# Kernel optimization log

Measured on AMD Instinct MI355X. Metric: run time of the kernel, lower is better.

## Reference

```python
import jax, jax.numpy as jnp
import numpy as np

N_EMBD = 384
N_HEAD = 6
HEAD_SIZE = N_EMBD // N_HEAD  # 64
B, T = 128, 256
EPS = 1e-5


def setup_inputs() -> dict:
    key = jax.random.key(0)
    ks = jax.random.split(key, 12)
    s = 0.02
    return {
        "x": jax.random.normal(ks[0], (B, T, N_EMBD), dtype=jnp.float32),
        "Wk": jax.random.normal(ks[1], (N_EMBD, N_EMBD), dtype=jnp.float32) * s,
        "Wq": jax.random.normal(ks[2], (N_EMBD, N_EMBD), dtype=jnp.float32) * s,
        "Wv": jax.random.normal(ks[3], (N_EMBD, N_EMBD), dtype=jnp.float32) * s,
        "Wo": jax.random.normal(ks[4], (N_EMBD, N_EMBD), dtype=jnp.float32) * s,
        "bo": jnp.zeros((N_EMBD,), dtype=jnp.float32),
        "W1": jax.random.normal(ks[5], (N_EMBD, 4 * N_EMBD), dtype=jnp.float32) * s,
        "b1": jnp.zeros((4 * N_EMBD,), dtype=jnp.float32),
        "W2": jax.random.normal(ks[6], (4 * N_EMBD, N_EMBD), dtype=jnp.float32) * s,
        "b2": jnp.zeros((N_EMBD,), dtype=jnp.float32),
        "g1": jnp.ones((N_EMBD,), dtype=jnp.float32),
        "be1": jnp.zeros((N_EMBD,), dtype=jnp.float32),
        "g2": jnp.ones((N_EMBD,), dtype=jnp.float32),
        "be2": jnp.zeros((N_EMBD,), dtype=jnp.float32),
    }


def _layernorm(x, g, b):
    mu = jnp.mean(x, axis=-1, keepdims=True)
    var = jnp.var(x, axis=-1, keepdims=True)
    return (x - mu) * jax.lax.rsqrt(var + EPS) * g + b


def _attention(x, Wk, Wq, Wv, Wo, bo):
    Bb, Tt, C = x.shape
    H, D = N_HEAD, HEAD_SIZE
    k = (x @ Wk).reshape(Bb, Tt, H, D).transpose(0, 2, 1, 3)  # (B,H,T,D)
    q = (x @ Wq).reshape(Bb, Tt, H, D).transpose(0, 2, 1, 3)
    v = (x @ Wv).reshape(Bb, Tt, H, D).transpose(0, 2, 1, 3)
    wei = jnp.einsum("bhqd,bhkd->bhqk", q, k) * (D ** -0.5)  # (B,H,T,T)
    mask = jnp.tril(jnp.ones((Tt, Tt), dtype=bool))
    wei = jnp.where(mask, wei, -jnp.inf)
    wei = jax.nn.softmax(wei, axis=-1)
    out = jnp.einsum("bhqk,bhkd->bhqd", wei, v)
    out = out.transpose(0, 2, 1, 3).reshape(Bb, Tt, H * D)
    return out @ Wo + bo


def reference(x, Wk, Wq, Wv, Wo, bo, W1, b1, W2, b2, g1, be1, g2, be2):
    # dropout is identity in eval mode
    h = _layernorm(x, g1, be1)
    x = x + _attention(h, Wk, Wq, Wv, Wo, bo)
    h = _layernorm(x, g2, be2)
    ff = jax.nn.relu(h @ W1 + b1) @ W2 + b2
    return x + ff
```

## Files before the change

### kernel.cpp

```cpp
#include <hip/hip_runtime.h>

typedef unsigned short u16;
typedef short s16x8 __attribute__((ext_vector_type(8)));
typedef float f32x4 __attribute__((ext_vector_type(4)));

__device__ inline u16 f2bf(float f) {
    unsigned u = __float_as_uint(f);
    u += 0x7FFF + ((u >> 16) & 1);
    return (u16)(u >> 16);
}
__device__ inline float bf2f(u16 h) {
    return __uint_as_float((unsigned)h << 16);
}

__device__ inline f32x4 mfma16(s16x8 a, s16x8 b, f32x4 c) {
    return __builtin_amdgcn_mfma_f32_16x16x32_bf16(a, b, c, 0, 0, 0);
}

__device__ __forceinline__ void gl16(const u16* g, u16* l) {
    __builtin_amdgcn_global_load_lds(
        (const __attribute__((address_space(1))) void*)g,
        (__attribute__((address_space(3))) void*)l, 16, 0, 0);
}

__global__ void tcvt_all(const float* __restrict__ Wq, const float* __restrict__ Wk,
                         const float* __restrict__ Wv, const float* __restrict__ Wo,
                         const float* __restrict__ W1, const float* __restrict__ W2,
                         u16* __restrict__ out) {
    int i = blockIdx.x * 256 + threadIdx.x;
    float val;
    if (i < 589824) {
        int q = i / 147456, j = i - q * 147456;
        const float* s = q == 0 ? Wq : q == 1 ? Wk : q == 2 ? Wv : Wo;
        int n = j / 384, k = j - n * 384;
        val = s[k * 384 + n];
    } else if (i < 1179648) {
        int j = i - 589824;
        int n = j / 384, k = j - n * 384;
        val = W1[(size_t)k * 1536 + n];
    } else {
        int j = i - 1179648;
        int n = j / 1536, k = j - n * 1536;
        val = W2[(size_t)k * 384 + n];
    }
    out[i] = f2bf(val);
}

__global__ __launch_bounds__(256) void ln_kernel(const float* __restrict__ x,
                                                 const float* __restrict__ g,
                                                 const float* __restrict__ be,
                                                 u16* __restrict__ out) {
    int lane = threadIdx.x & 63;
    int w = threadIdx.x >> 6;
    int row = blockIdx.x * 4 + w;
    const float* xr = x + (size_t)row * 384;
    float v[6];
    float s = 0.f, sq = 0.f;
#pragma unroll
    for (int i = 0; i < 6; ++i) {
        v[i] = xr[i * 64 + lane];
        s += v[i];
        sq += v[i] * v[i];
    }
#pragma unroll
    for (int m = 1; m < 64; m <<= 1) {
        s += __shfl_xor(s, m);
        sq += __shfl_xor(sq, m);
    }
    float mu = s * (1.0f / 384.0f);
    float var = sq * (1.0f / 384.0f) - mu * mu;
    float rstd = rsqrtf(var + 1e-5f);
    u16* orow = out + (size_t)row * 384;
#pragma unroll
    for (int i = 0; i < 6; ++i) {
        int col = i * 64 + lane;
        orow[col] = f2bf((v[i] - mu) * rstd * g[col] + be[col]);
    }
}

__global__ __launch_bounds__(256) void ln_bf16_kernel(const u16* __restrict__ x,
                                                      const float* __restrict__ g,
                                                      const float* __restrict__ be,
                                                      u16* __restrict__ out) {
    int lane = threadIdx.x & 63;
    int w = threadIdx.x >> 6;
    int row = blockIdx.x * 4 + w;
    const u16* xr = x + (size_t)row * 384;
    bool act = lane < 48;
    float v[8];
    float s = 0.f, sq = 0.f;
    if (act) {
        s16x8 t = *(const s16x8*)&xr[lane * 8];
#pragma unroll
        for (int j = 0; j < 8; ++j) {
            v[j] = bf2f((u16)t[j]);
            s += v[j];
            sq += v[j] * v[j];
        }
    }
#pragma unroll
    for (int m = 1; m < 64; m <<= 1) {
        s += __shfl_xor(s, m);
        sq += __shfl_xor(sq, m);
    }
    float mu = s * (1.0f / 384.0f);
    float var = sq * (1.0f / 384.0f) - mu * mu;
    float rstd = rsqrtf(var + 1e-5f);
    if (act) {
        float4 g0 = *(const float4*)&g[lane * 8];
        float4 g1 = *(const float4*)&g[lane * 8 + 4];
        float4 b0 = *(const float4*)&be[lane * 8];
        float4 b1 = *(const float4*)&be[lane * 8 + 4];
        float gg[8] = {g0.x, g0.y, g0.z, g0.w, g1.x, g1.y, g1.z, g1.w};
        float bb[8] = {b0.x, b0.y, b0.z, b0.w, b1.x, b1.y, b1.z, b1.w};
        u16* orow = out + (size_t)row * 384 + lane * 8;
#pragma unroll
        for (int j = 0; j < 8; ++j)
            orow[j] = f2bf((v[j] - mu) * rstd * gg[j] + bb[j]);
    }
}

template <int BIAS, int RELU, int RES, int RESBF, int OBF16, int NBN>
__global__ __launch_bounds__(512, 4) void gemm_kernel(const u16* __restrict__ A,
                                                      const u16* __restrict__ Bt,
                                                      const float* __restrict__ bias,
                                                      const void* __restrict__ res,
                                                      void* __restrict__ out,
                                                      int M, int N, int K) {
    __shared__ u16 La[2][256 * 32];
    __shared__ u16 Lb[2][128 * 32];
    int tid = threadIdx.x;
    int lane = tid & 63, w = tid >> 6;
    int wm = w >> 1, wn = w & 1;
    int lr = lane & 15, lg = lane >> 4;

    int nwg = gridDim.x;
    int q = nwg >> 3, r = nwg & 7;
    int xcd = blockIdx.x & 7, lin = blockIdx.x >> 3;
    int wg = (xcd < r ? xcd * (q + 1) : r * (q + 1) + (xcd - r) * q) + lin;
    int bx = wg % NBN, by = wg / NBN;
    int m0 = by * 256, n0 = bx * 128;

    int rsub = lane >> 2;
    int gslot = ((lane & 3) ^ ((lane >> 3) & 3)) * 8;
    const u16* pa[2];
    const u16* pb1;
#pragma unroll
    for (int i = 0; i < 2; ++i)
        pa[i] = A + (size_t)(m0 + w * 32 + i * 16 + rsub) * K + gslot;
    pb1 = Bt + (size_t)(n0 + w * 16 + rsub) * K + gslot;

    f32x4 acc[4][4];
    f32x4 zero = {0.f, 0.f, 0.f, 0.f};
#pragma unroll
    for (int mt = 0; mt < 4; ++mt)
#pragma unroll
        for (int nt = 0; nt < 4; ++nt) acc[mt][nt] = zero;

    int sel = (lg ^ ((lr >> 1) & 3)) << 3;
    int nt_steps = K >> 5;

#define STAGE(t, bsel)                                  \
    do {                                                \
        int kc = (t) << 5;                              \
        gl16(pa[0] + kc, &La[bsel][(w * 32) * 32]);     \
        gl16(pa[1] + kc, &La[bsel][(w * 32 + 16) * 32]);\
        gl16(pb1 + kc, &Lb[bsel][(w * 16) * 32]);       \
    } while (0)

    STAGE(0, 0);

    for (int t = 0; t < nt_steps; ++t) {
        asm volatile("s_waitcnt vmcnt(0)" ::: "memory");
        __builtin_amdgcn_s_barrier();
        asm volatile("" ::: "memory");
        if (t + 1 < nt_steps) STAGE(t + 1, (t + 1) & 1);
        const u16* lab = La[t & 1];
        const u16* lbb = Lb[t & 1];
        s16x8 af[4], bfr[4];
#pragma unroll
        for (int mt = 0; mt < 4; ++mt)
            af[mt] = *(const s16x8*)&lab[(wm * 64 + mt * 16 + lr) * 32 + sel];
#pragma unroll
        for (int nt = 0; nt < 4; ++nt)
            bfr[nt] = *(const s16x8*)&lbb[(wn * 64 + nt * 16 + lr) * 32 + sel];
        __builtin_amdgcn_s_setprio(1);
#pragma unroll
        for (int mt = 0; mt < 4; ++mt)
#pragma unroll
            for (int nt = 0; nt < 4; ++nt)
                acc[mt][nt] = mfma16(af[mt], bfr[nt], acc[mt][nt]);
        __builtin_amdgcn_s_setprio(0);
    }
#undef STAGE

#pragma unroll
    for (int mt = 0; mt < 4; ++mt) {
#pragma unroll
        for (int nt = 0; nt < 4; ++nt) {
            int m_base = m0 + wm * 64 + mt * 16 + lg * 4;
            int n = n0 + wn * 64 + nt * 16 + lr;
            float bv = BIAS ? bias[n] : 0.0f;
#pragma unroll
            for (int r2 = 0; r2 < 4; ++r2) {
                size_t idx = (size_t)(m_base + r2) * N + n;
                float val = acc[mt][nt][r2] + bv;
                if (RES) {
                    if (RESBF)
                        val += bf2f(((const u16*)res)[idx]);
                    else
                        val += ((const float*)res)[idx];
                }
                if (RELU) val = fmaxf(val, 0.0f);
                if (OBF16)
                    ((u16*)out)[idx] = f2bf(val);
                else
                    ((float*)out)[idx] = val;
            }
        }
    }
}

__global__ __launch_bounds__(512) void attn_kernel(const u16* __restrict__ qkv,
                                                   u16* __restrict__ aout) {
    __shared__ u16 Kl[256 * 72];
    __shared__ u16 Vt[64 * 264];
    __shared__ u16 Pl[8 * 16 * 264];
    int qt = blockIdx.x, h = blockIdx.y, b = blockIdx.z;
    int tid = threadIdx.x, lane = tid & 63, w = tid >> 6;
    int lr = lane & 15, lg = lane >> 4;
    const u16* qb = qkv + (size_t)b * 256 * 1152;

#pragma unroll
    for (int i = 0; i < 4; ++i) {
        int c = tid + i * 512;
        int t = c >> 3, dch = c & 7;
        *(int4*)&Kl[t * 72 + dch * 8] =
            *(const int4*)(qb + (size_t)t * 1152 + 384 + h * 64 + dch * 8);
        union { int4 v; u16 u[8]; } vv;
        vv.v = *(const int4*)(qb + (size_t)t * 1152 + 768 + h * 64 + dch * 8);
#pragma unroll
        for (int j = 0; j < 8; ++j) Vt[(dch * 8 + j) * 264 + t] = vv.u[j];
    }

    int q0 = qt * 128;
    const u16* qrow = qb + (size_t)(q0 + w * 16 + lr) * 1152 + h * 64;
    s16x8 qf0 = *(const s16x8*)(qrow + lg * 8);
    s16x8 qf1 = *(const s16x8*)(qrow + 32 + lg * 8);

    __syncthreads();

    f32x4 zero = {0.f, 0.f, 0.f, 0.f};
    f32x4 s[16];
#pragma unroll
    for (int nt = 0; nt < 16; ++nt) s[nt] = zero;
#pragma unroll
    for (int nt = 0; nt < 16; ++nt) {
        s16x8 kf0 = *(const s16x8*)&Kl[(nt * 16 + lr) * 72 + lg * 8];
        s16x8 kf1 = *(const s16x8*)&Kl[(nt * 16 + lr) * 72 + 32 + lg * 8];
        s[nt] = mfma16(qf0, kf0, s[nt]);
        s[nt] = mfma16(qf1, kf1, s[nt]);
    }

    int ib = q0 + w * 16 + lg * 4;
    float mx[4] = {-1e30f, -1e30f, -1e30f, -1e30f};
#pragma unroll
    for (int nt = 0; nt < 16; ++nt) {
        int jg = nt * 16 + lr;
#pragma unroll
        for (int r = 0; r < 4; ++r) {
            float val = s[nt][r] * 0.125f;
            val = (jg <= ib + r) ? val : -1e30f;
            s[nt][r] = val;
            mx[r] = fmaxf(mx[r], val);
        }
    }
#pragma unroll
    for (int r = 0; r < 4; ++r) {
        mx[r] = fmaxf(mx[r], __shfl_xor(mx[r], 1));
        mx[r] = fmaxf(mx[r], __shfl_xor(mx[r], 2));
        mx[r] = fmaxf(mx[r], __shfl_xor(mx[r], 4));
        mx[r] = fmaxf(mx[r], __shfl_xor(mx[r], 8));
    }
    float rs[4] = {0.f, 0.f, 0.f, 0.f};
#pragma unroll
    for (int nt = 0; nt < 16; ++nt) {
#pragma unroll
        for (int r = 0; r < 4; ++r) {
            float p = __expf(s[nt][r] - mx[r]);
            s[nt][r] = p;
            rs[r] += p;
        }
    }
#pragma unroll
    for (int r = 0; r < 4; ++r) {
        rs[r] += __shfl_xor(rs[r], 1);
        rs[r] += __shfl_xor(rs[r], 2);
        rs[r] += __shfl_xor(rs[r], 4);
        rs[r] += __shfl_xor(rs[r], 8);
    }
    u16* Pw = &Pl[w * 16 * 264];
#pragma unroll
    for (int nt = 0; nt < 16; ++nt)
#pragma unroll
        for (int r = 0; r < 4; ++r)
            Pw[(lg * 4 + r) * 264 + nt * 16 + lr] = f2bf(s[nt][r]);

    __syncthreads();

    f32x4 o[4];
#pragma unroll
    for (int nt = 0; nt < 4; ++nt) o[nt] = zero;
#pragma unroll
    for (int kc = 0; kc < 8; ++kc) {
        s16x8 pf = *(const s16x8*)&Pw[lr * 264 + kc * 32 + lg * 8];
#pragma unroll
        for (int nt = 0; nt < 4; ++nt) {
            s16x8 vf = *(const s16x8*)&Vt[(nt * 16 + lr) * 264 + kc * 32 + lg * 8];
            o[nt] = mfma16(pf, vf, o[nt]);
        }
    }
    float inv[4];
#pragma unroll
    for (int r = 0; r < 4; ++r) inv[r] = 1.0f / rs[r];
    u16* ob = aout + (size_t)(b * 256 + q0 + w * 16) * 384 + h * 64;
#pragma unroll
    for (int nt = 0; nt < 4; ++nt)
#pragma unroll
        for (int r = 0; r < 4; ++r)
            ob[(size_t)(lg * 4 + r) * 384 + nt * 16 + lr] = f2bf(o[nt][r] * inv[r]);
}

extern "C" void kernel_launch(void* const* d_in, const int* in_sizes, int n_in,
                              void* d_out, int out_size, void* d_ws, size_t ws_size,
                              hipStream_t stream) {
    const float* x   = (const float*)d_in[0];
    const float* Wk  = (const float*)d_in[1];
    const float* Wq  = (const float*)d_in[2];
    const float* Wv  = (const float*)d_in[3];
    const float* Wo  = (const float*)d_in[4];
    const float* bo  = (const float*)d_in[5];
    const float* W1  = (const float*)d_in[6];
    const float* b1  = (const float*)d_in[7];
    const float* W2  = (const float*)d_in[8];
    const float* b2  = (const float*)d_in[9];
    const float* g1  = (const float*)d_in[10];
    const float* be1 = (const float*)d_in[11];
    const float* g2  = (const float*)d_in[12];
    const float* be2 = (const float*)d_in[13];

    char* ws = (char*)d_ws;
    u16* hbuf = (u16*)(ws + 0);
    u16* qkv  = (u16*)(ws + 25165824);
    u16* ao   = (u16*)(ws + 100663296);
    u16* x1   = (u16*)(ws + 125829120);
    u16* ubuf = (u16*)(ws + 25165824);
    u16* wT   = (u16*)(ws + 150994944);
    u16* wqkvT = wT;
    u16* woT   = wT + 442368;
    u16* w1T   = woT + 147456;
    u16* w2T   = w1T + 589824;

    tcvt_all<<<6912, 256, 0, stream>>>(Wq, Wk, Wv, Wo, W1, W2, wT);

    ln_kernel<<<8192, 256, 0, stream>>>(x, g1, be1, hbuf);
    gemm_kernel<0, 0, 0, 0, 1, 9><<<1152, 512, 0, stream>>>(
        hbuf, wqkvT, nullptr, nullptr, qkv, 32768, 1152, 384);
    attn_kernel<<<dim3(2, 6, 128), 512, 0, stream>>>(qkv, ao);
    gemm_kernel<1, 0, 1, 0, 1, 3><<<384, 512, 0, stream>>>(
        ao, woT, bo, x, x1, 32768, 384, 384);
    ln_bf16_kernel<<<8192, 256, 0, stream>>>(x1, g2, be2, hbuf);
    gemm_kernel<1, 1, 0, 0, 1, 12><<<1536, 512, 0, stream>>>(
        hbuf, w1T, b1, nullptr, ubuf, 32768, 1536, 384);
    gemm_kernel<1, 0, 1, 1, 0, 3><<<384, 512, 0, stream>>>(
        ubuf, w2T, b2, x1, (float*)d_out, 32768, 384, 1536);
}
```

Before: 263.6 us.

## Split causal attention by query tile, skip masked keys, tile weight transpose

```diff
diff --git a/kernel.cpp b/kernel.cpp
--- a/kernel.cpp
+++ b/kernel.cpp
@@ -23,27 +23,42 @@
         (__attribute__((address_space(3))) void*)l, 16, 0, 0);
 }
 
-__global__ void tcvt_all(const float* __restrict__ Wq, const float* __restrict__ Wk,
-                         const float* __restrict__ Wv, const float* __restrict__ Wo,
-                         const float* __restrict__ W1, const float* __restrict__ W2,
-                         u16* __restrict__ out) {
-    int i = blockIdx.x * 256 + threadIdx.x;
-    float val;
-    if (i < 589824) {
-        int q = i / 147456, j = i - q * 147456;
-        const float* s = q == 0 ? Wq : q == 1 ? Wk : q == 2 ? Wv : Wo;
-        int n = j / 384, k = j - n * 384;
-        val = s[k * 384 + n];
-    } else if (i < 1179648) {
-        int j = i - 589824;
-        int n = j / 384, k = j - n * 384;
-        val = W1[(size_t)k * 1536 + n];
+__global__ __launch_bounds__(256) void tcvt_all(
+    const float* __restrict__ Wq, const float* __restrict__ Wk,
+    const float* __restrict__ Wv, const float* __restrict__ Wo,
+    const float* __restrict__ W1, const float* __restrict__ W2,
+    u16* __restrict__ wT) {
+    __shared__ float tile[32][33];
+    int bid = blockIdx.x;
+    const float* src;
+    u16* dst;
+    int K, N, tk, tn;
+    if (bid < 576) {
+        int m = bid / 144, t = bid - m * 144;
+        src = m == 0 ? Wq : m == 1 ? Wk : m == 2 ? Wv : Wo;
+        dst = wT + m * 147456;
+        K = 384; N = 384; tk = t / 12; tn = t - (t / 12) * 12;
+    } else if (bid < 1152) {
+        int t = bid - 576;
+        src = W1; dst = wT + 589824;
+        K = 384; N = 1536; tk = t / 48; tn = t - (t / 48) * 48;
     } else {
-        int j = i - 1179648;
-        int n = j / 1536, k = j - n * 1536;
-        val = W2[(size_t)k * 384 + n];
-    }
-    out[i] = f2bf(val);
+        int t = bid - 1152;
+        src = W2; dst = wT + 1179648;
+        K = 1536; N = 384; tk = t / 12; tn = t - (t / 12) * 12;
+    }
+    int tx = threadIdx.x & 31, ty = threadIdx.x >> 5;
+#pragma unroll
+    for (int p = 0; p < 4; ++p) {
+        int k = tk * 32 + ty + p * 8;
+        tile[ty + p * 8][tx] = src[(size_t)k * N + tn * 32 + tx];
+    }
+    __syncthreads();
+#pragma unroll
+    for (int p = 0; p < 4; ++p) {
+        int n = tn * 32 + ty + p * 8;
+        dst[(size_t)n * K + tk * 32 + tx] = f2bf(tile[tx][ty + p * 8]);
+    }
 }
 
 __global__ __launch_bounds__(256) void ln_kernel(const float* __restrict__ x,
@@ -221,18 +236,21 @@
     }
 }
 
+template <int QT0>
 __global__ __launch_bounds__(512) void attn_kernel(const u16* __restrict__ qkv,
                                                    u16* __restrict__ aout) {
     __shared__ u16 Kl[256 * 72];
     __shared__ u16 Vt[64 * 264];
     __shared__ u16 Pl[8 * 16 * 264];
-    int qt = blockIdx.x, h = blockIdx.y, b = blockIdx.z;
+    constexpr int NT = QT0 ? 8 : 16;
+    constexpr int NSTG = QT0 ? 2 : 4;
+    int h = blockIdx.x, b = blockIdx.y;
     int tid = threadIdx.x, lane = tid & 63, w = tid >> 6;
     int lr = lane & 15, lg = lane >> 4;
     const u16* qb = qkv + (size_t)b * 256 * 1152;
 
 #pragma unroll
-    for (int i = 0; i < 4; ++i) {
+    for (int i = 0; i < NSTG; ++i) {
         int c = tid + i * 512;
         int t = c >> 3, dch = c & 7;
         *(int4*)&Kl[t * 72 + dch * 8] =
@@ -243,7 +261,7 @@
         for (int j = 0; j < 8; ++j) Vt[(dch * 8 + j) * 264 + t] = vv.u[j];
     }
 
-    int q0 = qt * 128;
+    const int q0 = QT0 ? 0 : 128;
     const u16* qrow = qb + (size_t)(q0 + w * 16 + lr) * 1152 + h * 64;
     s16x8 qf0 = *(const s16x8*)(qrow + lg * 8);
     s16x8 qf1 = *(const s16x8*)(qrow + 32 + lg * 8);
@@ -251,11 +269,11 @@
     __syncthreads();
 
     f32x4 zero = {0.f, 0.f, 0.f, 0.f};
-    f32x4 s[16];
-#pragma unroll
-    for (int nt = 0; nt < 16; ++nt) s[nt] = zero;
-#pragma unroll
-    for (int nt = 0; nt < 16; ++nt) {
+    f32x4 s[NT];
+#pragma unroll
+    for (int nt = 0; nt < NT; ++nt) s[nt] = zero;
+#pragma unroll
+    for (int nt = 0; nt < NT; ++nt) {
         s16x8 kf0 = *(const s16x8*)&Kl[(nt * 16 + lr) * 72 + lg * 8];
         s16x8 kf1 = *(const s16x8*)&Kl[(nt * 16 + lr) * 72 + 32 + lg * 8];
         s[nt] = mfma16(qf0, kf0, s[nt]);
@@ -265,7 +283,7 @@
     int ib = q0 + w * 16 + lg * 4;
     float mx[4] = {-1e30f, -1e30f, -1e30f, -1e30f};
 #pragma unroll
-    for (int nt = 0; nt < 16; ++nt) {
+    for (int nt = 0; nt < NT; ++nt) {
         int jg = nt * 16 + lr;
 #pragma unroll
         for (int r = 0; r < 4; ++r) {
@@ -284,7 +302,7 @@
     }
     float rs[4] = {0.f, 0.f, 0.f, 0.f};
 #pragma unroll
-    for (int nt = 0; nt < 16; ++nt) {
+    for (int nt = 0; nt < NT; ++nt) {
 #pragma unroll
         for (int r = 0; r < 4; ++r) {
             float p = __expf(s[nt][r] - mx[r]);
@@ -301,18 +319,16 @@
     }
     u16* Pw = &Pl[w * 16 * 264];
 #pragma unroll
-    for (int nt = 0; nt < 16; ++nt)
+    for (int nt = 0; nt < NT; ++nt)
 #pragma unroll
         for (int r = 0; r < 4; ++r)
             Pw[(lg * 4 + r) * 264 + nt * 16 + lr] = f2bf(s[nt][r]);
 
-    __syncthreads();
-
     f32x4 o[4];
 #pragma unroll
     for (int nt = 0; nt < 4; ++nt) o[nt] = zero;
 #pragma unroll
-    for (int kc = 0; kc < 8; ++kc) {
+    for (int kc = 0; kc < NT / 2; ++kc) {
         s16x8 pf = *(const s16x8*)&Pw[lr * 264 + kc * 32 + lg * 8];
 #pragma unroll
         for (int nt = 0; nt < 4; ++nt) {
@@ -361,12 +377,13 @@
     u16* w1T   = woT + 147456;
     u16* w2T   = w1T + 589824;
 
-    tcvt_all<<<6912, 256, 0, stream>>>(Wq, Wk, Wv, Wo, W1, W2, wT);
+    tcvt_all<<<1728, 256, 0, stream>>>(Wq, Wk, Wv, Wo, W1, W2, wT);
 
     ln_kernel<<<8192, 256, 0, stream>>>(x, g1, be1, hbuf);
     gemm_kernel<0, 0, 0, 0, 1, 9><<<1152, 512, 0, stream>>>(
         hbuf, wqkvT, nullptr, nullptr, qkv, 32768, 1152, 384);
-    attn_kernel<<<dim3(2, 6, 128), 512, 0, stream>>>(qkv, ao);
+    attn_kernel<1><<<dim3(6, 128), 512, 0, stream>>>(qkv, ao);
+    attn_kernel<0><<<dim3(6, 128), 512, 0, stream>>>(qkv, ao);
     gemm_kernel<1, 0, 1, 0, 1, 3><<<384, 512, 0, stream>>>(
         ao, woT, bo, x, x1, 32768, 384, 384);
     ln_bf16_kernel<<<8192, 256, 0, stream>>>(x1, g2, be2, hbuf);
```

Result: faster. 249.4 us (-5.4%).
